# Kernel optimization log

Measured on AMD Instinct MI355X. Metric: run time of the kernel, lower is better.

The kernel has to match this reference:

```python
import jax, jax.numpy as jnp
import numpy as np

TOKENS, D_IN, D_OUT, N_FACTORS, RANK = 8192, 4096, 4096, 2, 64


def setup_inputs() -> dict:
    key = jax.random.key(0)
    ks = jax.random.split(key, 6)
    # kaiming_uniform-ish scales (exact init distribution is irrelevant for correctness)
    w_bound = 1.0 / np.sqrt(D_IN)
    x = jax.random.normal(ks[0], (TOKENS, D_IN), dtype=jnp.float32)
    W = jax.random.uniform(ks[1], (D_OUT, D_IN), jnp.float32, -w_bound, w_bound)
    bias = jax.random.uniform(ks[2], (D_OUT,), jnp.float32, -w_bound, w_bound)
    a_bound = 1.0 / np.sqrt(RANK)
    As = jax.random.uniform(ks[3], (N_FACTORS, D_OUT, RANK), jnp.float32, -a_bound, a_bound)
    Bs = jax.random.normal(ks[4], (N_FACTORS, RANK, RANK), dtype=jnp.float32) * 0.1
    # Cs initialized nonzero here so the low-rank path actually contributes
    Cs = jax.random.normal(ks[5], (N_FACTORS, RANK, D_IN), dtype=jnp.float32) * 0.02
    return {"x": x, "W": W, "bias": bias, "As": As, "Bs": Bs, "Cs": Cs}


def reference(x, W, bias, As, Bs, Cs):
    # W_eff = W + sum_f tanh(A_f) @ B_f @ C_f   (phi_A = tanh, B already transformed)
    # [f,o,r] x [f,r,k] -> [f,o,k]; then x [f,k,i] -> [o,i] summed over f
    AB = jnp.einsum('for,frk->fok', jnp.tanh(As), Bs)
    W_eff = W + jnp.einsum('fok,fki->oi', AB, Cs)
    # F.linear: x @ W_eff^T + bias
    return jnp.einsum('ti,oi->to', x, W_eff) + bias
```

## Files before the change

kernel.cpp:

```cpp
#include <hip/hip_runtime.h>
#include <hip/hip_bf16.h>

typedef __bf16 bf16x8 __attribute__((ext_vector_type(8)));
typedef float f32x4 __attribute__((ext_vector_type(4)));

#define TOKENS 8192
#define D_IN   4096
#define D_OUT  4096

static __device__ __forceinline__ unsigned short f2bf(float f) {
  union { float f; unsigned int u; } v; v.f = f;
  unsigned int r = v.u + 0x7FFFu + ((v.u >> 16) & 1u);
  return (unsigned short)(r >> 16);
}

__global__ void ab_kernel(const float* __restrict__ As,
                          const float* __restrict__ Bs,
                          float* __restrict__ ABt) {
  __shared__ float tA[4][64];
  __shared__ float sB[64][64];
  const int t = threadIdx.x;
  const int f = blockIdx.x >> 10;
  const int o0 = (blockIdx.x & 1023) * 4;
  const int ol = t >> 6;
  const int k  = t & 63;
  tA[ol][k] = tanhf(As[((size_t)f * 4096 + o0 + ol) * 64 + k]);
#pragma unroll
  for (int j = 0; j < 16; ++j) {
    int e = t + 256 * j;
    sB[e >> 6][e & 63] = Bs[f * 4096 + e];
  }
  __syncthreads();
  float acc = 0.f;
#pragma unroll
  for (int r = 0; r < 64; ++r) acc += tA[ol][r] * sB[r][k];
  ABt[(size_t)(o0 + ol) * 128 + f * 64 + k] = acc;
}

__global__ void weff_kernel(const float* __restrict__ W,
                            const float* __restrict__ ABt,
                            const float* __restrict__ Cs,
                            unsigned short* __restrict__ Weff) {
  __shared__ float sA[64][129];
  __shared__ float sB[32][64];
  const int t = threadIdx.x;
  const int i0 = blockIdx.x * 64;
  const int o0 = blockIdx.y * 64;
#pragma unroll
  for (int j = 0; j < 32; ++j) {
    int e = t + 256 * j;
    sA[e >> 7][e & 127] = ABt[(size_t)(o0 + (e >> 7)) * 128 + (e & 127)];
  }
  const int tx = t & 15, ty = t >> 4;
  float acc[4][4] = {};
  for (int kc = 0; kc < 128; kc += 32) {
    __syncthreads();
#pragma unroll
    for (int j = 0; j < 8; ++j) {
      int e = t + 256 * j;
      sB[e >> 6][e & 63] = Cs[(size_t)(kc + (e >> 6)) * D_IN + i0 + (e & 63)];
    }
    __syncthreads();
#pragma unroll
    for (int k = 0; k < 32; ++k) {
      float4 b = *(const float4*)&sB[k][tx * 4];
#pragma unroll
      for (int r = 0; r < 4; ++r) {
        float a = sA[ty * 4 + r][kc + k];
        acc[r][0] += a * b.x;
        acc[r][1] += a * b.y;
        acc[r][2] += a * b.z;
        acc[r][3] += a * b.w;
      }
    }
  }
#pragma unroll
  for (int r = 0; r < 4; ++r) {
    const int o = o0 + ty * 4 + r;
    const float4 w = *(const float4*)&W[(size_t)o * D_IN + i0 + tx * 4];
    union { unsigned short h[4]; uint2 u; } p;
    p.h[0] = f2bf(w.x + acc[r][0]);
    p.h[1] = f2bf(w.y + acc[r][1]);
    p.h[2] = f2bf(w.z + acc[r][2]);
    p.h[3] = f2bf(w.w + acc[r][3]);
    *(uint2*)(Weff + (size_t)o * D_IN + i0 + tx * 4) = p.u;
  }
}

__global__ void cast_kernel(const float* __restrict__ x,
                            unsigned short* __restrict__ xb) {
  size_t i = ((size_t)blockIdx.x * 256 + threadIdx.x) * 8;
  float4 a = *(const float4*)(x + i);
  float4 b = *(const float4*)(x + i + 4);
  union { unsigned short h[8]; uint4 u; } p;
  p.h[0] = f2bf(a.x); p.h[1] = f2bf(a.y);
  p.h[2] = f2bf(a.z); p.h[3] = f2bf(a.w);
  p.h[4] = f2bf(b.x); p.h[5] = f2bf(b.y);
  p.h[6] = f2bf(b.z); p.h[7] = f2bf(b.w);
  *(uint4*)(xb + i) = p.u;
}


#define FENCE()   asm volatile("" ::: "memory")
#define BARRIER() do { FENCE(); __builtin_amdgcn_s_barrier(); FENCE(); } while (0)
#define WAITVM(n)  asm volatile("s_waitcnt vmcnt(" #n ")" ::: "memory")
#define SCHEDB()   __builtin_amdgcn_sched_barrier(0)
#define PRIO1      __builtin_amdgcn_s_setprio(1)
#define PRIO0      __builtin_amdgcn_s_setprio(0)

#define GLOAD(gptr, lptr)                                                     \
  __builtin_amdgcn_global_load_lds(                                           \
      (const __attribute__((address_space(1))) void*)(gptr),                  \
      (__attribute__((address_space(3))) void*)(lptr), 16, 0, 0)

#define STAGE_A(buf, h, kt) do {                                              \
    GLOAD(ag + (size_t)((h) * 128) * K + (kt),                                \
          lA + (buf) * 16384 + (h) * 8192);                                   \
    GLOAD(ag + (size_t)((h) * 128 + 64) * K + (kt),                           \
          lA + (buf) * 16384 + (h) * 8192 + 4096);                            \
  } while (0)
#define STAGE_B(buf, h, kt) do {                                              \
    GLOAD(bg + (size_t)((h) * 128) * K + (kt),                                \
          lB + (buf) * 16384 + (h) * 8192);                                   \
    GLOAD(bg + (size_t)((h) * 128 + 64) * K + (kt),                           \
          lB + (buf) * 16384 + (h) * 8192 + 4096);                            \
  } while (0)

#define LDA(buf, mi, ks) \
  (*(const bf16x8*)(rA + (buf) * 16384 + (mi) * 1024 + ((ks) ? ch1 : ch0)))
#define LDB(buf, ni, ks) \
  (*(const bf16x8*)(rB + (buf) * 16384 + (ni) * 1024 + ((ks) ? ch1 : ch0)))

#define READ_A(R0, R1, R2, R3, buf, mi0) do {                                 \
    R0 = LDA(buf, (mi0), 0);                                                  \
    R2 = LDA(buf, (mi0) + 1, 0);                                              \
    R1 = LDA(buf, (mi0), 1);                                                  \
    R3 = LDA(buf, (mi0) + 1, 1);                                              \
  } while (0)
#define READ_B(buf) do {                                                      \
    b00 = LDB(buf, 0, 0); b10 = LDB(buf, 1, 0);                               \
    b20 = LDB(buf, 2, 0); b30 = LDB(buf, 3, 0);                               \
    b01 = LDB(buf, 0, 1); b11 = LDB(buf, 1, 1);                               \
    b21 = LDB(buf, 2, 1); b31 = LDB(buf, 3, 1);                               \
  } while (0)

#define MFMA1(d, a, b) \
  (d) = __builtin_amdgcn_mfma_f32_16x16x32_bf16((a), (b), (d), 0, 0, 0)

#define QUAD(q, A0, A1, A2, A3)                                               \
    MFMA1(acc[2*(q)  ][0], A0, b00);                                          \
    MFMA1(acc[2*(q)+1][0], A2, b00);                                          \
    MFMA1(acc[2*(q)  ][1], A0, b10);                                          \
    MFMA1(acc[2*(q)+1][1], A2, b10);                                          \
    MFMA1(acc[2*(q)  ][2], A0, b20);                                          \
    MFMA1(acc[2*(q)+1][2], A2, b20);                                          \
    MFMA1(acc[2*(q)  ][3], A0, b30);                                          \
    MFMA1(acc[2*(q)+1][3], A2, b30);                                          \
    MFMA1(acc[2*(q)  ][0], A1, b01);                                          \
    MFMA1(acc[2*(q)+1][0], A3, b01);                                          \
    MFMA1(acc[2*(q)  ][1], A1, b11);                                          \
    MFMA1(acc[2*(q)+1][1], A3, b11);                                          \
    MFMA1(acc[2*(q)  ][2], A1, b21);                                          \
    MFMA1(acc[2*(q)+1][2], A3, b21);                                          \
    MFMA1(acc[2*(q)  ][3], A1, b31);                                          \
    MFMA1(acc[2*(q)+1][3], A3, b31);

#define GEMM_BODY(S2, S3, kt)                                                 \
  {                                                                           \
                             \
    READ_B(0);                                                                \
    READ_A(qa0, qa1, qa2, qa3, 0, 2);                                         \
    STAGE_A(1, 0, (kt) + 64); STAGE_A(1, 1, (kt) + 64);                       \
    BARRIER(); SCHEDB();                                                      \
    PRIO1; QUAD(0, pa0, pa1, pa2, pa3); PRIO0; SCHEDB();                      \
    BARRIER();                                                                \
                                          \
    READ_A(pa0, pa1, pa2, pa3, 0, 4);                                         \
    if (S2) { STAGE_B(0, 0, (kt) + 128); STAGE_B(0, 1, (kt) + 128); }         \
    BARRIER(); SCHEDB();                                                      \
    PRIO1; QUAD(1, qa0, qa1, qa2, qa3); PRIO0; SCHEDB();                      \
    BARRIER();                                                                \
                         \
    READ_A(qa0, qa1, qa2, qa3, 0, 6);                                         \
    BARRIER(); SCHEDB();                                                      \
    PRIO1; QUAD(2, pa0, pa1, pa2, pa3); PRIO0; SCHEDB();                      \
    if (S2) { WAITVM(4); } else { WAITVM(0); }                                \
    BARRIER();                                                                \
                                  \
    READ_A(pa0, pa1, pa2, pa3, 1, 0);                                         \
    BARRIER(); SCHEDB();                                                      \
    PRIO1; QUAD(3, qa0, qa1, qa2, qa3); PRIO0; SCHEDB();                      \
    BARRIER();                                                                \
                               \
    READ_B(1);                                                                \
    READ_A(qa0, qa1, qa2, qa3, 1, 2);                                         \
    if (S2) { STAGE_A(0, 0, (kt) + 128); STAGE_A(0, 1, (kt) + 128); }         \
    BARRIER(); SCHEDB();                                                      \
    PRIO1; QUAD(0, pa0, pa1, pa2, pa3); PRIO0; SCHEDB();                      \
    BARRIER();                                                                \
                                        \
    READ_A(pa0, pa1, pa2, pa3, 1, 4);                                         \
    if (S3) { STAGE_B(1, 0, (kt) + 192); STAGE_B(1, 1, (kt) + 192); }         \
    BARRIER(); SCHEDB();                                                      \
    PRIO1; QUAD(1, qa0, qa1, qa2, qa3); PRIO0; SCHEDB();                      \
    BARRIER();                                                                \
                       \
    READ_A(qa0, qa1, qa2, qa3, 1, 6);                                         \
    BARRIER(); SCHEDB();                                                      \
    PRIO1; QUAD(2, pa0, pa1, pa2, pa3); PRIO0; SCHEDB();                      \
    if (S3) { WAITVM(4); } else { WAITVM(0); }                                \
    BARRIER();                                                                \
                                  \
    if (S2) { READ_A(pa0, pa1, pa2, pa3, 0, 0); }                             \
    BARRIER(); SCHEDB();                                                      \
    PRIO1; QUAD(3, qa0, qa1, qa2, qa3); PRIO0; SCHEDB();                      \
    BARRIER();                                                                \
  }

__global__ __launch_bounds__(512, 2) void gemm_kernel(
    const unsigned short* __restrict__ Abf,
    const unsigned short* __restrict__ Bbf,
    const float* __restrict__ bias,
    float* __restrict__ C) {
  const int K = D_IN, N = D_OUT;
  __shared__ __align__(16) unsigned short sA[2 * 256 * 64];
  __shared__ __align__(16) unsigned short sB[2 * 256 * 64];
  const int t = threadIdx.x;
  const int lane = t & 63;
  const int wave = t >> 6;

  const int wgid = blockIdx.y * gridDim.x + blockIdx.x;
  const int swz = (wgid & 7) * 64 + (wgid >> 3);
  const int bn = swz & 15;
  const int bm = swz >> 4;

  const int wm = (wave >> 2) * 128;
  const int wn = (wave & 3) * 64;

  const int tr = t >> 3;
  const int cg = (t & 7) ^ (tr & 7);
  const unsigned short* ag = Abf + (size_t)(bm * 256 + tr) * K + cg * 8;
  const unsigned short* bg = Bbf + (size_t)(bn * 256 + tr) * K + cg * 8;
  unsigned short* const lA = sA + t * 8;
  unsigned short* const lB = sB + t * 8;

  const int lm = lane & 15;
  const int cb = lane >> 4;
  const int sw = lm & 7;
  const int ch0 = ((cb) ^ sw) * 8;
  const int ch1 = ((4 + cb) ^ sw) * 8;
  const unsigned short* rA = sA + (wm + lm) * 64;
  const unsigned short* rB = sB + (wn + lm) * 64;

  f32x4 acc[8][4] = {};
  bf16x8 pa0, pa1, pa2, pa3;
  bf16x8 qa0, qa1, qa2, qa3;
  bf16x8 b00, b10, b20, b30, b01, b11, b21, b31;

  STAGE_B(0, 0, 0); STAGE_B(0, 1, 0);
  STAGE_A(0, 0, 0); STAGE_A(0, 1, 0);
  STAGE_B(1, 0, 64); STAGE_B(1, 1, 64);
  WAITVM(4);
  BARRIER();
  READ_A(pa0, pa1, pa2, pa3, 0, 0);

#pragma unroll 1
  for (int kt = 0; kt < K - 128; kt += 128) GEMM_BODY(1, 1, kt)
  GEMM_BODY(0, 0, K - 128)

  const int cn = lane & 15;
  const int rm = (lane >> 4) * 4;
#pragma unroll
  for (int ni = 0; ni < 4; ++ni) {
    const int col = bn * 256 + wn + ni * 16 + cn;
    const float bv = bias[col];
#pragma unroll
    for (int mi = 0; mi < 8; ++mi) {
      const int row0 = bm * 256 + wm + mi * 16 + rm;
#pragma unroll
      for (int r = 0; r < 4; ++r)
        C[(size_t)(row0 + r) * N + col] = acc[mi][ni][r] + bv;
    }
  }
}

extern "C" void kernel_launch(void* const* d_in, const int* in_sizes, int n_in,
                              void* d_out, int out_size, void* d_ws, size_t ws_size,
                              hipStream_t stream) {
  const float* x    = (const float*)d_in[0];
  const float* W    = (const float*)d_in[1];
  const float* bias = (const float*)d_in[2];
  const float* As   = (const float*)d_in[3];
  const float* Bs   = (const float*)d_in[4];
  const float* Cs   = (const float*)d_in[5];
  float* out = (float*)d_out;

  char* ws = (char*)d_ws;
  float* ABt           = (float*)ws;
  unsigned short* Weff = (unsigned short*)(ws + (2u << 20));
  unsigned short* xb   = (unsigned short*)(ws + (2u << 20) + (32u << 20));

  ab_kernel<<<2048, 256, 0, stream>>>(As, Bs, ABt);
  weff_kernel<<<dim3(64, 64), 256, 0, stream>>>(W, ABt, Cs, Weff);
  cast_kernel<<<16384, 256, 0, stream>>>(x, xb);
  gemm_kernel<<<dim3(16, 32), 512, 0, stream>>>(xb, Weff, bias, out);
}
```

Baseline: 565.5 us.

## Double-buffer B fragments in registers and spread LDS reads across sub-phases

Replaces the single set of B register fragments with two alternating sets (pb/qb), so B fragments for the next half-tile are read from LDS one column-group per phase, interleaved with the A reads, rather than all at once. Global-to-LDS staging is also rescheduled: B and A stages are split into halves spread across phases, A for the next tile is prefetched in the prologue, and the vmcnt waits are adjusted. The goal is to smooth LDS read and global load traffic so that MFMA issue stalls less. The cost is eight extra bf16x8 registers per thread, which may pressure occupancy at launch bounds (512,2), and the hand-tuned waitcnt values carry a risk of races.

```diff
diff --git a/kernel.cpp b/kernel.cpp
--- a/kernel.cpp
+++ b/kernel.cpp
@@ -137,84 +137,104 @@
     R1 = LDA(buf, (mi0), 1);                                                  \
     R3 = LDA(buf, (mi0) + 1, 1);                                              \
   } while (0)
-#define READ_B(buf) do {                                                      \
-    b00 = LDB(buf, 0, 0); b10 = LDB(buf, 1, 0);                               \
-    b20 = LDB(buf, 2, 0); b30 = LDB(buf, 3, 0);                               \
-    b01 = LDB(buf, 0, 1); b11 = LDB(buf, 1, 1);                               \
-    b21 = LDB(buf, 2, 1); b31 = LDB(buf, 3, 1);                               \
+#define READ_B1(Bp, buf, ni) do {                                             \
+    Bp##ni##0 = LDB(buf, ni, 0);                                              \
+    Bp##ni##1 = LDB(buf, ni, 1);                                              \
   } while (0)
 
 #define MFMA1(d, a, b) \
   (d) = __builtin_amdgcn_mfma_f32_16x16x32_bf16((a), (b), (d), 0, 0, 0)
 
-#define QUAD(q, A0, A1, A2, A3)                                               \
-    MFMA1(acc[2*(q)  ][0], A0, b00);                                          \
-    MFMA1(acc[2*(q)+1][0], A2, b00);                                          \
-    MFMA1(acc[2*(q)  ][1], A0, b10);                                          \
-    MFMA1(acc[2*(q)+1][1], A2, b10);                                          \
-    MFMA1(acc[2*(q)  ][2], A0, b20);                                          \
-    MFMA1(acc[2*(q)+1][2], A2, b20);                                          \
-    MFMA1(acc[2*(q)  ][3], A0, b30);                                          \
-    MFMA1(acc[2*(q)+1][3], A2, b30);                                          \
-    MFMA1(acc[2*(q)  ][0], A1, b01);                                          \
-    MFMA1(acc[2*(q)+1][0], A3, b01);                                          \
-    MFMA1(acc[2*(q)  ][1], A1, b11);                                          \
-    MFMA1(acc[2*(q)+1][1], A3, b11);                                          \
-    MFMA1(acc[2*(q)  ][2], A1, b21);                                          \
-    MFMA1(acc[2*(q)+1][2], A3, b21);                                          \
-    MFMA1(acc[2*(q)  ][3], A1, b31);                                          \
-    MFMA1(acc[2*(q)+1][3], A3, b31);
+#define PBSET pb00, pb10, pb20, pb30, pb01, pb11, pb21, pb31
+#define QBSET qb00, qb10, qb20, qb30, qb01, qb11, qb21, qb31
+#define QUAD(...) QUAD_I(__VA_ARGS__)
+#define QUAD_I(q, A0, A1, A2, A3, B00, B10, B20, B30, B01, B11, B21, B31)     \
+    MFMA1(acc[2*(q)  ][0], A0, B00);                                          \
+    MFMA1(acc[2*(q)+1][0], A2, B00);                                          \
+    MFMA1(acc[2*(q)  ][1], A0, B10);                                          \
+    MFMA1(acc[2*(q)+1][1], A2, B10);                                          \
+    MFMA1(acc[2*(q)  ][2], A0, B20);                                          \
+    MFMA1(acc[2*(q)+1][2], A2, B20);                                          \
+    MFMA1(acc[2*(q)  ][3], A0, B30);                                          \
+    MFMA1(acc[2*(q)+1][3], A2, B30);                                          \
+    MFMA1(acc[2*(q)  ][0], A1, B01);                                          \
+    MFMA1(acc[2*(q)+1][0], A3, B01);                                          \
+    MFMA1(acc[2*(q)  ][1], A1, B11);                                          \
+    MFMA1(acc[2*(q)+1][1], A3, B11);                                          \
+    MFMA1(acc[2*(q)  ][2], A1, B21);                                          \
+    MFMA1(acc[2*(q)+1][2], A3, B21);                                          \
+    MFMA1(acc[2*(q)  ][3], A1, B31);                                          \
+    MFMA1(acc[2*(q)+1][3], A3, B31);
 
 #define GEMM_BODY(S2, S3, kt)                                                 \
   {                                                                           \
-                             \
-    READ_B(0);                                                                \
-    READ_A(qa0, qa1, qa2, qa3, 0, 2);                                         \
-    STAGE_A(1, 0, (kt) + 64); STAGE_A(1, 1, (kt) + 64);                       \
-    BARRIER(); SCHEDB();                                                      \
-    PRIO1; QUAD(0, pa0, pa1, pa2, pa3); PRIO0; SCHEDB();                      \
-    BARRIER();                                                                \
-                                          \
-    READ_A(pa0, pa1, pa2, pa3, 0, 4);                                         \
-    if (S2) { STAGE_B(0, 0, (kt) + 128); STAGE_B(0, 1, (kt) + 128); }         \
-    BARRIER(); SCHEDB();                                                      \
-    PRIO1; QUAD(1, qa0, qa1, qa2, qa3); PRIO0; SCHEDB();                      \
-    BARRIER();                                                                \
-                         \
-    READ_A(qa0, qa1, qa2, qa3, 0, 6);                                         \
-    BARRIER(); SCHEDB();                                                      \
-    PRIO1; QUAD(2, pa0, pa1, pa2, pa3); PRIO0; SCHEDB();                      \
-    if (S2) { WAITVM(4); } else { WAITVM(0); }                                \
-    BARRIER();                                                                \
-                                  \
-    READ_A(pa0, pa1, pa2, pa3, 1, 0);                                         \
-    BARRIER(); SCHEDB();                                                      \
-    PRIO1; QUAD(3, qa0, qa1, qa2, qa3); PRIO0; SCHEDB();                      \
-    BARRIER();                                                                \
-                               \
-    READ_B(1);                                                                \
-    READ_A(qa0, qa1, qa2, qa3, 1, 2);                                         \
-    if (S2) { STAGE_A(0, 0, (kt) + 128); STAGE_A(0, 1, (kt) + 128); }         \
-    BARRIER(); SCHEDB();                                                      \
-    PRIO1; QUAD(0, pa0, pa1, pa2, pa3); PRIO0; SCHEDB();                      \
-    BARRIER();                                                                \
-                                        \
-    READ_A(pa0, pa1, pa2, pa3, 1, 4);                                         \
-    if (S3) { STAGE_B(1, 0, (kt) + 192); STAGE_B(1, 1, (kt) + 192); }         \
-    BARRIER(); SCHEDB();                                                      \
-    PRIO1; QUAD(1, qa0, qa1, qa2, qa3); PRIO0; SCHEDB();                      \
-    BARRIER();                                                                \
-                       \
-    READ_A(qa0, qa1, qa2, qa3, 1, 6);                                         \
-    BARRIER(); SCHEDB();                                                      \
-    PRIO1; QUAD(2, pa0, pa1, pa2, pa3); PRIO0; SCHEDB();                      \
-    if (S3) { WAITVM(4); } else { WAITVM(0); }                                \
-    BARRIER();                                                                \
-                                  \
-    if (S2) { READ_A(pa0, pa1, pa2, pa3, 0, 0); }                             \
-    BARRIER(); SCHEDB();                                                      \
-    PRIO1; QUAD(3, qa0, qa1, qa2, qa3); PRIO0; SCHEDB();                      \
-    BARRIER();                                                                \
+    {                 \
+      READ_A(qa0, qa1, qa2, qa3, 0, 2);                                       \
+      READ_B1(qb, 1, 0);                                                      \
+      if (S2) STAGE_B(0, 0, (kt) + 128);                                      \
+      BARRIER(); SCHEDB();                                                    \
+      PRIO1; QUAD(0, pa0, pa1, pa2, pa3, PBSET); PRIO0; SCHEDB();             \
+      BARRIER();                                                              \
+    }                                                                         \
+    {                 \
+      READ_A(pa0, pa1, pa2, pa3, 0, 4);                                       \
+      READ_B1(qb, 1, 1);                                                      \
+      if (S2) STAGE_B(0, 1, (kt) + 128);                                      \
+      BARRIER(); SCHEDB();                                                    \
+      PRIO1; QUAD(1, qa0, qa1, qa2, qa3, PBSET); PRIO0; SCHEDB();             \
+      BARRIER();                                                              \
+    }                                                                         \
+    {                 \
+      READ_A(qa0, qa1, qa2, qa3, 0, 6);                                       \
+      READ_B1(qb, 1, 2);                                                      \
+      BARRIER(); SCHEDB();                                                    \
+      PRIO1; QUAD(2, pa0, pa1, pa2, pa3, PBSET); PRIO0; SCHEDB();             \
+      if (S2) { WAITVM(4); } else { WAITVM(0); }                              \
+      BARRIER();                                                              \
+    }                                                                         \
+    {   \
+      READ_A(pa0, pa1, pa2, pa3, 1, 0);                                       \
+      READ_B1(qb, 1, 3);                                                      \
+      if (S2) STAGE_A(0, 0, (kt) + 128);                                      \
+      BARRIER(); SCHEDB();                                                    \
+      PRIO1; QUAD(3, qa0, qa1, qa2, qa3, PBSET); PRIO0; SCHEDB();             \
+      if (S2) { WAITVM(2); }                                                  \
+      BARRIER();                                                              \
+    }                                                                         \
+    {   \
+      READ_A(qa0, qa1, qa2, qa3, 1, 2);                                       \
+      if (S2) READ_B1(pb, 0, 0);                                              \
+      if (S2) STAGE_A(0, 1, (kt) + 128);                                      \
+      if (S3) STAGE_B(1, 0, (kt) + 192);                                      \
+      BARRIER(); SCHEDB();                                                    \
+      PRIO1; QUAD(0, pa0, pa1, pa2, pa3, QBSET); PRIO0; SCHEDB();             \
+      BARRIER();                                                              \
+    }                                                                         \
+    {             \
+      READ_A(pa0, pa1, pa2, pa3, 1, 4);                                       \
+      if (S2) READ_B1(pb, 0, 1);                                              \
+      if (S3) STAGE_B(1, 1, (kt) + 192);                                      \
+      BARRIER(); SCHEDB();                                                    \
+      PRIO1; QUAD(1, qa0, qa1, qa2, qa3, QBSET); PRIO0; SCHEDB();             \
+      BARRIER();                                                              \
+    }                                                                         \
+    {             \
+      READ_A(qa0, qa1, qa2, qa3, 1, 6);                                       \
+      if (S2) READ_B1(pb, 0, 2);                                              \
+      BARRIER(); SCHEDB();                                                    \
+      PRIO1; QUAD(2, pa0, pa1, pa2, pa3, QBSET); PRIO0; SCHEDB();             \
+      if (S2) { WAITVM(4); }                                                  \
+      BARRIER();                                                              \
+    }                                                                         \
+    {   \
+      if (S2) READ_A(pa0, pa1, pa2, pa3, 0, 0);                               \
+      if (S2) READ_B1(pb, 0, 3);                                              \
+      if (S3) { STAGE_A(1, 0, (kt) + 192); STAGE_A(1, 1, (kt) + 192); }       \
+      BARRIER(); SCHEDB();                                                    \
+      PRIO1; QUAD(3, qa0, qa1, qa2, qa3, QBSET); PRIO0; SCHEDB();             \
+      if (S3) { WAITVM(4); }                                                  \
+      BARRIER();                                                              \
+    }                                                                         \
   }
 
 __global__ __launch_bounds__(512, 2) void gemm_kernel(
@@ -255,13 +275,17 @@
   f32x4 acc[8][4] = {};
   bf16x8 pa0, pa1, pa2, pa3;
   bf16x8 qa0, qa1, qa2, qa3;
-  bf16x8 b00, b10, b20, b30, b01, b11, b21, b31;
+  bf16x8 PBSET;
+  bf16x8 QBSET;
 
   STAGE_B(0, 0, 0); STAGE_B(0, 1, 0);
   STAGE_A(0, 0, 0); STAGE_A(0, 1, 0);
   STAGE_B(1, 0, 64); STAGE_B(1, 1, 64);
+  STAGE_A(1, 0, 64); STAGE_A(1, 1, 64);
   WAITVM(4);
   BARRIER();
+  READ_B1(pb, 0, 0); READ_B1(pb, 0, 1);
+  READ_B1(pb, 0, 2); READ_B1(pb, 0, 3);
   READ_A(pa0, pa1, pa2, pa3, 0, 0);
 
 #pragma unroll 1
```

Result: slower. 623.7 us (+10.3%).

## Compute W_eff low-rank update with bf16 MFMA using transposed bf16 Cs

Applied to the files above, without the earlier changes.

The low-rank correction AB@C is now computed with bf16 MFMA instructions instead of fp32 scalar FMAs. AB is stored as bf16, and Cs is transposed and cast to bf16 in an extra branch of the x-cast kernel so both operands are K-contiguous for the MFMA layout. Operands are staged with direct global-to-LDS loads into swizzled tiles. This reduces ALU time in weff_kernel, but rounding AB and C to bf16 adds precision loss, and the epilogue now does scalar rather than vectorized W reads and Weff writes.

```diff
diff --git a/kernel.cpp b/kernel.cpp
--- a/kernel.cpp
+++ b/kernel.cpp
@@ -16,7 +16,7 @@
 
 __global__ void ab_kernel(const float* __restrict__ As,
                           const float* __restrict__ Bs,
-                          float* __restrict__ ABt) {
+                          unsigned short* __restrict__ ABt) {
   __shared__ float tA[4][64];
   __shared__ float sB[64][64];
   const int t = threadIdx.x;
@@ -34,70 +34,117 @@
   float acc = 0.f;
 #pragma unroll
   for (int r = 0; r < 64; ++r) acc += tA[ol][r] * sB[r][k];
-  ABt[(size_t)(o0 + ol) * 128 + f * 64 + k] = acc;
-}
-
-__global__ void weff_kernel(const float* __restrict__ W,
-                            const float* __restrict__ ABt,
+  ABt[(size_t)(o0 + ol) * 128 + f * 64 + k] = f2bf(acc);
+}
+
+__global__ void cast_kernel(const float* __restrict__ x,
+                            unsigned short* __restrict__ xb,
                             const float* __restrict__ Cs,
-                            unsigned short* __restrict__ Weff) {
-  __shared__ float sA[64][129];
-  __shared__ float sB[32][64];
+                            unsigned short* __restrict__ Cst) {
+  __shared__ float tp[64][65];
   const int t = threadIdx.x;
-  const int i0 = blockIdx.x * 64;
-  const int o0 = blockIdx.y * 64;
-#pragma unroll
-  for (int j = 0; j < 32; ++j) {
-    int e = t + 256 * j;
-    sA[e >> 7][e & 127] = ABt[(size_t)(o0 + (e >> 7)) * 128 + (e & 127)];
-  }
-  const int tx = t & 15, ty = t >> 4;
-  float acc[4][4] = {};
-  for (int kc = 0; kc < 128; kc += 32) {
+  if (blockIdx.x < 16384) {
+    size_t i = ((size_t)blockIdx.x * 256 + t) * 8;
+    float4 a = *(const float4*)(x + i);
+    float4 b = *(const float4*)(x + i + 4);
+    union { unsigned short h[8]; uint4 u; } p;
+    p.h[0] = f2bf(a.x); p.h[1] = f2bf(a.y);
+    p.h[2] = f2bf(a.z); p.h[3] = f2bf(a.w);
+    p.h[4] = f2bf(b.x); p.h[5] = f2bf(b.y);
+    p.h[6] = f2bf(b.z); p.h[7] = f2bf(b.w);
+    *(uint4*)(xb + i) = p.u;
+  } else {
+    const int b2 = blockIdx.x - 16384;
+    const int k0 = (b2 & 1) * 64;
+    const int i0 = (b2 >> 1) * 64;
+#pragma unroll
+    for (int j = 0; j < 16; ++j) {
+      int e = t + 256 * j;
+      tp[e >> 6][e & 63] = Cs[(size_t)(k0 + (e >> 6)) * 4096 + i0 + (e & 63)];
+    }
     __syncthreads();
 #pragma unroll
-    for (int j = 0; j < 8; ++j) {
+    for (int j = 0; j < 16; ++j) {
       int e = t + 256 * j;
-      sB[e >> 6][e & 63] = Cs[(size_t)(kc + (e >> 6)) * D_IN + i0 + (e & 63)];
-    }
+      Cst[(size_t)(i0 + (e >> 6)) * 128 + k0 + (e & 63)] =
+          f2bf(tp[e & 63][e >> 6]);
+    }
+  }
+}
+
+__global__ __launch_bounds__(256) void weff_kernel(
+    const float* __restrict__ W,
+    const unsigned short* __restrict__ ABt,
+    const unsigned short* __restrict__ Cst,
+    unsigned short* __restrict__ Weff) {
+  const int KW = 128;
+  __shared__ __align__(16) unsigned short sA[128 * 64];
+  __shared__ __align__(16) unsigned short sB[128 * 64];
+  const int t = threadIdx.x;
+  const int lane = t & 63;
+  const int wave = t >> 6;
+  const int bi = blockIdx.x, bo = blockIdx.y;
+  const int wm = (wave & 1) * 64, wn = (wave >> 1) * 64;
+
+  const int tr = t >> 3;
+  const int cg = (t & 7) ^ (tr & 7);
+  const unsigned short* agA = ABt + (size_t)(bo * 128 + tr) * KW + cg * 8;
+  const unsigned short* agB = Cst + (size_t)(bi * 128 + tr) * KW + cg * 8;
+  unsigned short* const la = sA + t * 8;
+  unsigned short* const lb = sB + t * 8;
+
+  f32x4 acc[4][4] = {};
+  const int lm = lane & 15;
+  const int cb = lane >> 4;
+  const int sw = lm & 7;
+
+  for (int kt = 0; kt < KW; kt += 64) {
     __syncthreads();
 #pragma unroll
-    for (int k = 0; k < 32; ++k) {
-      float4 b = *(const float4*)&sB[k][tx * 4];
+    for (int j = 0; j < 4; ++j) {
+      __builtin_amdgcn_global_load_lds(
+          (const __attribute__((address_space(1))) void*)(agA + (size_t)j * 32 * KW + kt),
+          (__attribute__((address_space(3))) void*)(la + j * 2048), 16, 0, 0);
+      __builtin_amdgcn_global_load_lds(
+          (const __attribute__((address_space(1))) void*)(agB + (size_t)j * 32 * KW + kt),
+          (__attribute__((address_space(3))) void*)(lb + j * 2048), 16, 0, 0);
+    }
+    __syncthreads();
+#pragma unroll
+    for (int ks = 0; ks < 2; ++ks) {
+      const int ch = ((ks * 4 + cb) ^ sw) * 8;
+      bf16x8 af[4], bfr[4];
+#pragma unroll
+      for (int mi = 0; mi < 4; ++mi)
+        af[mi] = *(const bf16x8*)(sA + (wm + mi * 16 + lm) * 64 + ch);
+#pragma unroll
+      for (int ni = 0; ni < 4; ++ni)
+        bfr[ni] = *(const bf16x8*)(sB + (wn + ni * 16 + lm) * 64 + ch);
+#pragma unroll
+      for (int mi = 0; mi < 4; ++mi)
+#pragma unroll
+        for (int ni = 0; ni < 4; ++ni)
+          acc[mi][ni] = __builtin_amdgcn_mfma_f32_16x16x32_bf16(
+              af[mi], bfr[ni], acc[mi][ni], 0, 0, 0);
+    }
+  }
+
+  const int cn = lane & 15;
+  const int rm = (lane >> 4) * 4;
+#pragma unroll
+  for (int ni = 0; ni < 4; ++ni) {
+    const int col = bi * 128 + wn + ni * 16 + cn;
+#pragma unroll
+    for (int mi = 0; mi < 4; ++mi) {
+      const int row0 = bo * 128 + wm + mi * 16 + rm;
 #pragma unroll
       for (int r = 0; r < 4; ++r) {
-        float a = sA[ty * 4 + r][kc + k];
-        acc[r][0] += a * b.x;
-        acc[r][1] += a * b.y;
-        acc[r][2] += a * b.z;
-        acc[r][3] += a * b.w;
+        const int row = row0 + r;
+        Weff[(size_t)row * D_IN + col] =
+            f2bf(W[(size_t)row * D_IN + col] + acc[mi][ni][r]);
       }
     }
   }
-#pragma unroll
-  for (int r = 0; r < 4; ++r) {
-    const int o = o0 + ty * 4 + r;
-    const float4 w = *(const float4*)&W[(size_t)o * D_IN + i0 + tx * 4];
-    union { unsigned short h[4]; uint2 u; } p;
-    p.h[0] = f2bf(w.x + acc[r][0]);
-    p.h[1] = f2bf(w.y + acc[r][1]);
-    p.h[2] = f2bf(w.z + acc[r][2]);
-    p.h[3] = f2bf(w.w + acc[r][3]);
-    *(uint2*)(Weff + (size_t)o * D_IN + i0 + tx * 4) = p.u;
-  }
-}
-
-__global__ void cast_kernel(const float* __restrict__ x,
-                            unsigned short* __restrict__ xb) {
-  size_t i = ((size_t)blockIdx.x * 256 + threadIdx.x) * 8;
-  float4 a = *(const float4*)(x + i);
-  float4 b = *(const float4*)(x + i + 4);
-  union { unsigned short h[8]; uint4 u; } p;
-  p.h[0] = f2bf(a.x); p.h[1] = f2bf(a.y);
-  p.h[2] = f2bf(a.z); p.h[3] = f2bf(a.w);
-  p.h[4] = f2bf(b.x); p.h[5] = f2bf(b.y);
-  p.h[6] = f2bf(b.z); p.h[7] = f2bf(b.w);
-  *(uint4*)(xb + i) = p.u;
 }
 
 
@@ -296,12 +343,13 @@
   float* out = (float*)d_out;
 
   char* ws = (char*)d_ws;
-  float* ABt           = (float*)ws;
+  unsigned short* ABt  = (unsigned short*)ws;
+  unsigned short* Cst  = (unsigned short*)(ws + (1u << 20));
   unsigned short* Weff = (unsigned short*)(ws + (2u << 20));
   unsigned short* xb   = (unsigned short*)(ws + (2u << 20) + (32u << 20));
 
   ab_kernel<<<2048, 256, 0, stream>>>(As, Bs, ABt);
-  weff_kernel<<<dim3(64, 64), 256, 0, stream>>>(W, ABt, Cs, Weff);
-  cast_kernel<<<16384, 256, 0, stream>>>(x, xb);
+  cast_kernel<<<16384 + 128, 256, 0, stream>>>(x, xb, Cs, Cst);
+  weff_kernel<<<dim3(32, 32), 256, 0, stream>>>(W, ABt, Cst, Weff);
   gemm_kernel<<<dim3(16, 32), 512, 0, stream>>>(xb, Weff, bias, out);
 }
```

Result: no change. 556.5 us (-1.6%).
